# Performance work log

Hardware: AMD Instinct MI355X
Metric: run time of the kernel (lower is better)

## Reference

```python
import jax, jax.numpy as jnp
import numpy as np

B, T, F, H = 1024, 512, 32, 64
EPS = 1e-3  # keras BatchNormalization default epsilon


def lstm_layer(x, Wx, Uh, b):
    """Keras LSTM with activation=relu, recurrent_activation=sigmoid.
    x: [B,T,Fin]; Wx: [Fin,4H]; Uh: [H,4H]; b: [4H]. Gate order i,f,c,o."""
    xz = jnp.einsum('btf,fg->btg', x, Wx) + b  # precompute input projection
    h0 = jnp.zeros((x.shape[0], Uh.shape[0]), x.dtype)

    def step(carry, xz_t):
        h, c = carry
        z = xz_t + h @ Uh
        i, f, g, o = jnp.split(z, 4, axis=-1)
        i = jax.nn.sigmoid(i)
        f = jax.nn.sigmoid(f)
        o = jax.nn.sigmoid(o)
        c = f * c + i * jax.nn.relu(g)
        h = o * jax.nn.relu(c)
        return (h, c), h

    _, hs = jax.lax.scan(step, (h0, h0), jnp.swapaxes(xz, 0, 1))  # [T,B,H]
    return jnp.swapaxes(hs, 0, 1)  # [B,T,H]


def batchnorm(x, gamma, beta, mean, var):
    # inference-mode BN over last axis (keras default axis=-1, training=False)
    return (x - mean) * (gamma * jax.lax.rsqrt(var + EPS)) + beta


def attention(x, W, ht):
    # score = (X @ W) @ h_t -> [B,T]; softmax over time; c_t = X^T @ alpha
    score = jnp.einsum('btd,de,e->bt', x, W, ht[:, 0])
    alpha = jax.nn.softmax(score, axis=1)
    return jnp.einsum('btd,bt->bd', x, alpha)  # [B,H]


def setup_inputs() -> dict:
    key = jax.random.key(0)
    ks = jax.random.split(key, 32)
    d = {'x': jax.random.normal(ks[0], (B, T, F), jnp.float32)}
    fins = [F, H, H]
    for l in range(3):
        fin = fins[l]
        i = l + 1
        d[f'w{i}'] = jax.random.normal(ks[1 + 9 * l], (fin, 4 * H), jnp.float32) * (1.0 / np.sqrt(fin))
        d[f'u{i}'] = jax.random.normal(ks[2 + 9 * l], (H, 4 * H), jnp.float32) * (1.0 / np.sqrt(H))
        d[f'bi{i}'] = jnp.zeros((4 * H,), jnp.float32)
        d[f'gamma{i}'] = jnp.ones((H,), jnp.float32)
        d[f'beta{i}'] = jnp.zeros((H,), jnp.float32)
        d[f'mean{i}'] = jax.random.normal(ks[3 + 9 * l], (H,), jnp.float32) * 0.1
        d[f'var{i}'] = jnp.ones((H,), jnp.float32) + jax.random.uniform(ks[4 + 9 * l], (H,), jnp.float32) * 0.1
        d[f'attw{i}'] = jax.random.truncated_normal(ks[5 + 9 * l], -2, 2, (H, H), jnp.float32) * 0.5
        d[f'attv{i}'] = jax.random.truncated_normal(ks[6 + 9 * l], -2, 2, (H, 1), jnp.float32) * 0.5
    d['dw'] = jax.random.normal(ks[30], (3 * H, 1), jnp.float32) * (1.0 / np.sqrt(3 * H))
    d['db'] = jnp.zeros((1,), jnp.float32)
    return d


def reference(x, w1, u1, bi1, gamma1, beta1, mean1, var1, attw1, attv1,
              w2, u2, bi2, gamma2, beta2, mean2, var2, attw2, attv2,
              w3, u3, bi3, gamma3, beta3, mean3, var3, attw3, attv3,
              dw, db):
    h = lstm_layer(x, w1, u1, bi1)
    h = batchnorm(h, gamma1, beta1, mean1, var1)
    a1 = attention(h, attw1, attv1)
    h = lstm_layer(h, w2, u2, bi2)
    h = batchnorm(h, gamma2, beta2, mean2, var2)
    a2 = attention(h, attw2, attv2)
    h = lstm_layer(h, w3, u3, bi3)
    h = batchnorm(h, gamma3, beta3, mean3, var3)
    a3 = attention(h, attw3, attv3)
    feat = jnp.concatenate([a1, a2, a3], axis=1)  # [B, 3H]
    return feat @ dw + db  # [B, 1]
```

## Files before the change

### kernel.cpp

```cpp
#include <hip/hip_runtime.h>
#include <math.h>

#define BB 1024
#define TT 512
#define FF 32
#define HH 64
#define GG 256
#define TC 64
#define NCHUNK (TT/TC)
#define MB 16
#define NBLK (BB/MB)
#define HPAD 68
#define EPSBN 1e-3f

typedef __attribute__((ext_vector_type(8))) short bf16x8;
typedef __attribute__((ext_vector_type(4))) float f32x4;
typedef __attribute__((ext_vector_type(4))) int   i32x4;

__global__ void fold1_kernel(const float* __restrict__ gamma, const float* __restrict__ beta,
                             const float* __restrict__ mean, const float* __restrict__ var,
                             const float* __restrict__ attw, const float* __restrict__ attv,
                             float* __restrict__ s_out, float* __restrict__ ab_out,
                             float* __restrict__ wv_out) {
    int d = threadIdx.x;
    float s = gamma[d] * rsqrtf(var[d] + EPSBN);
    float ab = beta[d] - mean[d] * s;
    float wvr = 0.f;
    for (int e = 0; e < HH; ++e) wvr += attw[d * HH + e] * attv[e];
    s_out[d] = s;
    ab_out[d] = ab;
    wv_out[d] = s * wvr;
}

__global__ void fold2_kernel(const float* __restrict__ W, const float* __restrict__ b,
                             const float* __restrict__ s_prev, const float* __restrict__ ab_prev,
                             float* __restrict__ Wp, float* __restrict__ bp) {
    int g = threadIdx.x;
    float bacc = b[g];
    for (int d = 0; d < HH; ++d) {
        float w = W[d * GG + g];
        bacc += ab_prev[d] * w;
        Wp[d * GG + g] = s_prev[d] * w;
    }
    bp[g] = bacc;
}

__global__ void init_kernel(float* st_h, float* st_c, float* st_acc, float* st_m, float* st_d) {
    int i = blockIdx.x * blockDim.x + threadIdx.x;
    int n = 3 * BB * HH;
    if (i < n) { st_h[i] = 0.f; st_c[i] = 0.f; st_acc[i] = 0.f; }
    if (i < 3 * BB) { st_m[i] = -3.0e38f; st_d[i] = 0.f; }
}

__device__ __forceinline__ f32x4 ld4(const float* p) { return *reinterpret_cast<const f32x4*>(p); }
__device__ __forceinline__ void st4(float* p, f32x4 v) { *reinterpret_cast<f32x4*>(p) = v; }
__device__ __forceinline__ int cvtpk(float a, float b) {
    int r; asm("v_cvt_pk_bf16_f32 %0, %1, %2" : "=v"(r) : "v"(a), "v"(b)); return r;
}
__device__ __forceinline__ void mkfrag(f32x4 A, f32x4 B, bf16x8& hi, bf16x8& lo) {
    i32x4 H, L;
    H[0] = cvtpk(A[0], A[1]); H[1] = cvtpk(A[2], A[3]);
    H[2] = cvtpk(B[0], B[1]); H[3] = cvtpk(B[2], B[3]);
    L[0] = cvtpk(A[0] - __int_as_float(H[0] << 16), A[1] - __int_as_float(H[0] & 0xffff0000));
    L[1] = cvtpk(A[2] - __int_as_float(H[1] << 16), A[3] - __int_as_float(H[1] & 0xffff0000));
    L[2] = cvtpk(B[0] - __int_as_float(H[2] << 16), B[1] - __int_as_float(H[2] & 0xffff0000));
    L[3] = cvtpk(B[2] - __int_as_float(H[3] << 16), B[3] - __int_as_float(H[3] & 0xffff0000));
    hi = __builtin_bit_cast(bf16x8, H); lo = __builtin_bit_cast(bf16x8, L);
}
__device__ __forceinline__ float sigm(float x) { return __fdividef(1.f, 1.f + __expf(-x)); }
#define MFMA(a, b, c) c = __builtin_amdgcn_mfma_f32_16x16x32_bf16(a, b, c, 0, 0, 0)

struct RecFArgs {
    const float* xin[3]; long sB[3]; long sT[3]; int K[3];
    const float* W[3]; const float* U[3]; const float* bias[3];
    float* Hout[3];
    float* st_h[3]; float* st_c[3]; float* st_acc[3];
    float* st_m[3]; float* st_d[3];
    const float* wv[3]; const float* abv[3]; const float* sbn[3];
    float* a_out[3];
    int last[3]; int first[3];
};

template<int KT>
__device__ __forceinline__ void rec_body(const RecFArgs& A, const int seg, const int b0,
                                         float (*hl)[MB][HPAD]) {
    const int tid = threadIdx.x;
    const int w = tid >> 6;
    const int l = tid & 63;
    const int r = l & 15;
    const int q = l >> 4;
    const int cw = w << 4;

    bf16x8 UHf[4][2], ULf[4][2], WHf[4][KT], WLf[4][KT];
    {
        const float* Up = A.U[seg];
#pragma unroll
        for (int g = 0; g < 4; ++g)
#pragma unroll
            for (int kk = 0; kk < 2; ++kk) {
                const float* p = Up + (size_t)(32 * kk + 8 * q) * GG + 64 * g + cw + r;
                f32x4 a, b;
                a[0] = p[0];      a[1] = p[GG];     a[2] = p[2 * GG]; a[3] = p[3 * GG];
                b[0] = p[4 * GG]; b[1] = p[5 * GG]; b[2] = p[6 * GG]; b[3] = p[7 * GG];
                mkfrag(a, b, UHf[g][kk], ULf[g][kk]);
            }
        const float* Wp = A.W[seg];
#pragma unroll
        for (int g = 0; g < 4; ++g)
#pragma unroll
            for (int kk = 0; kk < KT; ++kk) {
                const float* p = Wp + (size_t)(32 * kk + 8 * q) * GG + 64 * g + cw + r;
                f32x4 a, b;
                a[0] = p[0];      a[1] = p[GG];     a[2] = p[2 * GG]; a[3] = p[3 * GG];
                b[0] = p[4 * GG]; b[1] = p[5 * GG]; b[2] = p[6 * GG]; b[3] = p[7 * GG];
                mkfrag(a, b, WHf[g][kk], WLf[g][kk]);
            }
    }
    f32x4 bias4[4];
#pragma unroll
    for (int g = 0; g < 4; ++g) bias4[g] = ld4(A.bias[seg] + 64 * g + cw + 4 * q);

    f32x4 wva = ld4(A.wv[seg] + 8 * q);
    f32x4 wvb = ld4(A.wv[seg] + 8 * q + 4);
    f32x4 wvc = ld4(A.wv[seg] + 32 + 8 * q);
    f32x4 wvd = ld4(A.wv[seg] + 32 + 8 * q + 4);

    const int grow = b0 + r;
    f32x4 c4   = ld4(A.st_c[seg]   + (size_t)grow * HH + cw + 4 * q);
    f32x4 h4   = ld4(A.st_h[seg]   + (size_t)grow * HH + cw + 4 * q);
    f32x4 acc4 = ld4(A.st_acc[seg] + (size_t)grow * HH + cw + 4 * q);
    float m_b = A.st_m[seg][grow];
    float d_b = A.st_d[seg][grow];

    st4(&hl[0][r][cw + 4 * q], h4);

    const float* xbase = A.xin[seg] + (size_t)grow * A.sB[seg];
    const long sT = A.sT[seg];

    f32x4 XA[2 * KT], XB[2 * KT];
    auto xload = [&](f32x4 (&X)[2 * KT], int t) {
        const float* xp = xbase + (size_t)t * sT + 8 * q;
        X[0] = ld4(xp); X[1] = ld4(xp + 4);
        if constexpr (KT == 2) { X[2] = ld4(xp + 32); X[3] = ld4(xp + 32 + 4); }
    };
    xload(XA, 0);
    xload(XB, 1);

    f32x4 Ca[4], Cb[4];
    auto seedC = [&](f32x4 (&C)[4], f32x4 (&X)[2 * KT]) {
        bf16x8 xh0, xl0, xh1, xl1;
        mkfrag(X[0], X[1], xh0, xl0);
        if constexpr (KT == 2) mkfrag(X[2], X[3], xh1, xl1);
#pragma unroll
        for (int g = 0; g < 4; ++g) {
            C[g] = bias4[g];
            MFMA(WHf[g][0], xh0, C[g]);
            MFMA(WHf[g][0], xl0, C[g]);
            MFMA(WLf[g][0], xh0, C[g]);
            if constexpr (KT == 2) {
                MFMA(WHf[g][1], xh1, C[g]);
                MFMA(WHf[g][1], xl1, C[g]);
                MFMA(WLf[g][1], xh1, C[g]);
            }
        }
    };

    auto attup = [&](int pr) {
        f32x4 f0 = ld4(&hl[pr][r][8 * q]);
        f32x4 f1 = ld4(&hl[pr][r][8 * q + 4]);
        f32x4 f2 = ld4(&hl[pr][r][32 + 8 * q]);
        f32x4 f3 = ld4(&hl[pr][r][32 + 8 * q + 4]);
        float sc = 0.f;
#pragma unroll
        for (int i = 0; i < 4; ++i) {
            sc = fmaf(f0[i], wva[i], sc);
            sc = fmaf(f1[i], wvb[i], sc);
            sc = fmaf(f2[i], wvc[i], sc);
            sc = fmaf(f3[i], wvd[i], sc);
        }
        sc += __shfl_xor(sc, 16);
        sc += __shfl_xor(sc, 32);
        float mn = fmaxf(m_b, sc);
        float corr = __expf(m_b - mn);
        float p = __expf(sc - mn);
        d_b = d_b * corr + p;
        acc4 = acc4 * corr + p * h4;
        m_b = mn;
    };

    float* Hob = A.Hout[seg];
    auto step = [&](int t, f32x4 (&C)[4], int pr, bool do_att) {
        if (Hob && w == 3 && t > 0) {
            const int sr = l >> 2, scol = (l & 3) << 4;
            f32x4 v0 = ld4(&hl[pr][sr][scol]);
            f32x4 v1 = ld4(&hl[pr][sr][scol + 4]);
            f32x4 v2 = ld4(&hl[pr][sr][scol + 8]);
            f32x4 v3 = ld4(&hl[pr][sr][scol + 12]);
            float* op = Hob + (size_t)(b0 + sr) * (TC * HH) + (size_t)(t - 1) * HH + scol;
            st4(op, v0); st4(op + 4, v1); st4(op + 8, v2); st4(op + 12, v3);
        }
        if (do_att) attup(pr);
        f32x4 f0 = ld4(&hl[pr][r][8 * q]);
        f32x4 f1 = ld4(&hl[pr][r][8 * q + 4]);
        f32x4 f2 = ld4(&hl[pr][r][32 + 8 * q]);
        f32x4 f3 = ld4(&hl[pr][r][32 + 8 * q + 4]);
        bf16x8 bh0, bl0, bh1, bl1;
        mkfrag(f0, f1, bh0, bl0);
        mkfrag(f2, f3, bh1, bl1);
#pragma unroll
        for (int g = 0; g < 4; ++g) {
            MFMA(UHf[g][0], bh0, C[g]);
            MFMA(UHf[g][0], bl0, C[g]);
            MFMA(ULf[g][0], bh0, C[g]);
            MFMA(UHf[g][1], bh1, C[g]);
            MFMA(UHf[g][1], bl1, C[g]);
            MFMA(ULf[g][1], bh1, C[g]);
        }
#pragma unroll
        for (int i = 0; i < 4; ++i) {
            float zi = sigm(C[0][i]);
            float zf = sigm(C[1][i]);
            float zg = fmaxf(C[2][i], 0.f);
            float zo = sigm(C[3][i]);
            c4[i] = fmaf(zf, c4[i], zi * zg);
            h4[i] = zo * fmaxf(c4[i], 0.f);
        }
        st4(&hl[pr ^ 1][r][cw + 4 * q], h4);
    };

    const bool first = (A.first[seg] != 0);
    seedC(Ca, XA);
    __syncthreads();

#pragma unroll 1
    for (int it = 0; it < TC / 2; ++it) {
        const int t0 = 2 * it, t1 = 2 * it + 1;
        step(t0, Ca, 0, !(first && t0 == 0));
        xload(XA, (t0 + 2 < TC) ? t0 + 2 : TC - 1);
        seedC(Cb, XB);
        __syncthreads();
        step(t1, Cb, 1, true);
        xload(XB, (t1 + 2 < TC) ? t1 + 2 : TC - 1);
        seedC(Ca, XA);
        __syncthreads();
    }

    if (Hob && w == 3) {
        const int sr = l >> 2, scol = (l & 3) << 4;
        f32x4 v0 = ld4(&hl[0][sr][scol]);
        f32x4 v1 = ld4(&hl[0][sr][scol + 4]);
        f32x4 v2 = ld4(&hl[0][sr][scol + 8]);
        f32x4 v3 = ld4(&hl[0][sr][scol + 12]);
        float* op = Hob + (size_t)(b0 + sr) * (TC * HH) + (size_t)(TC - 1) * HH + scol;
        st4(op, v0); st4(op + 4, v1); st4(op + 8, v2); st4(op + 12, v3);
    }
    if (A.last[seg]) {
        attup(0);
        f32x4 sb = ld4(A.sbn[seg] + cw + 4 * q);
        f32x4 ab = ld4(A.abv[seg] + cw + 4 * q);
        f32x4 res;
#pragma unroll
        for (int i = 0; i < 4; ++i)
            res[i] = sb[i] * __fdividef(acc4[i], d_b) + ab[i];
        st4(A.a_out[seg] + (size_t)grow * HH + cw + 4 * q, res);
    }
    st4(A.st_c[seg]   + (size_t)grow * HH + cw + 4 * q, c4);
    st4(A.st_h[seg]   + (size_t)grow * HH + cw + 4 * q, h4);
    st4(A.st_acc[seg] + (size_t)grow * HH + cw + 4 * q, acc4);
    if (w == 0 && q == 0) { A.st_m[seg][grow] = m_b; A.st_d[seg][grow] = d_b; }
}

__global__ __launch_bounds__(256, 1) void rec_mfma(RecFArgs A) {
    __shared__ float hl[2][MB][HPAD];
    const int seg = blockIdx.x >> 6;
    const int b0 = (blockIdx.x & (NBLK - 1)) << 4;
    if (A.K[seg] == 32) rec_body<1>(A, seg, b0, hl);
    else                rec_body<2>(A, seg, b0, hl);
}

__global__ void final_kernel(const float* __restrict__ a, const float* __restrict__ dw,
                             const float* __restrict__ db, float* __restrict__ out) {
    int b = blockIdx.x * blockDim.x + threadIdx.x;
    if (b >= BB) return;
    float acc = db[0];
    for (int l = 0; l < 3; ++l)
        for (int j = 0; j < HH; ++j)
            acc += a[(l * BB + b) * HH + j] * dw[l * HH + j];
    out[b] = acc;
}

extern "C" void kernel_launch(void* const* d_in, const int* in_sizes, int n_in,
                              void* d_out, int out_size, void* d_ws, size_t ws_size,
                              hipStream_t stream) {
    (void)in_sizes; (void)n_in; (void)out_size; (void)ws_size;
    const float* x = (const float*)d_in[0];
    const float* w[3]    = {(const float*)d_in[1],  (const float*)d_in[10], (const float*)d_in[19]};
    const float* uu[3]   = {(const float*)d_in[2],  (const float*)d_in[11], (const float*)d_in[20]};
    const float* bi[3]   = {(const float*)d_in[3],  (const float*)d_in[12], (const float*)d_in[21]};
    const float* gam[3]  = {(const float*)d_in[4],  (const float*)d_in[13], (const float*)d_in[22]};
    const float* bet[3]  = {(const float*)d_in[5],  (const float*)d_in[14], (const float*)d_in[23]};
    const float* mea[3]  = {(const float*)d_in[6],  (const float*)d_in[15], (const float*)d_in[24]};
    const float* var[3]  = {(const float*)d_in[7],  (const float*)d_in[16], (const float*)d_in[25]};
    const float* atw[3]  = {(const float*)d_in[8],  (const float*)d_in[17], (const float*)d_in[26]};
    const float* atv[3]  = {(const float*)d_in[9],  (const float*)d_in[18], (const float*)d_in[27]};
    const float* dw = (const float*)d_in[28];
    const float* db = (const float*)d_in[29];

    float* ws = (float*)d_ws;
    size_t off = 0;
    float* Hb[2][2];
    for (int l = 0; l < 2; ++l)
        for (int p = 0; p < 2; ++p) { Hb[l][p] = ws + off; off += (size_t)BB * TC * HH; }
    float* st_h  = ws + off; off += 3 * BB * HH;
    float* st_c  = ws + off; off += 3 * BB * HH;
    float* st_ac = ws + off; off += 3 * BB * HH;
    float* st_m  = ws + off; off += 3 * BB;
    float* st_d  = ws + off; off += 3 * BB;
    float* s_ws  = ws + off; off += 3 * HH;
    float* ab_ws = ws + off; off += 3 * HH;
    float* wv_ws = ws + off; off += 3 * HH;
    float* W2p   = ws + off; off += HH * GG;
    float* W3p   = ws + off; off += HH * GG;
    float* b2p   = ws + off; off += GG;
    float* b3p   = ws + off; off += GG;
    float* a_ws  = ws + off; off += 3 * BB * HH;

    for (int l = 0; l < 3; ++l)
        fold1_kernel<<<1, 64, 0, stream>>>(gam[l], bet[l], mea[l], var[l], atw[l], atv[l],
                                           s_ws + l * HH, ab_ws + l * HH, wv_ws + l * HH);
    fold2_kernel<<<1, 256, 0, stream>>>(w[1], bi[1], s_ws + 0 * HH, ab_ws + 0 * HH, W2p, b2p);
    fold2_kernel<<<1, 256, 0, stream>>>(w[2], bi[2], s_ws + 1 * HH, ab_ws + 1 * HH, W3p, b3p);
    init_kernel<<<(3 * BB * HH + 255) / 256, 256, 0, stream>>>(st_h, st_c, st_ac, st_m, st_d);

    const float* Wl[3] = {w[0], W2p, W3p};
    const float* bl[3] = {bi[0], b2p, b3p};

    for (int s = 0; s <= NCHUNK - 1 + 2; ++s) {
        RecFArgs ra;
        int nseg = 0;
        for (int l = 0; l < 3; ++l) {
            int cpos = s - l;
            if (cpos < 0 || cpos >= NCHUNK) continue;
            if (l == 0) {
                ra.xin[nseg] = x + (size_t)cpos * TC * FF;
                ra.sB[nseg] = (long)TT * FF;
                ra.sT[nseg] = FF;
                ra.K[nseg] = 32;
            } else {
                ra.xin[nseg] = Hb[l - 1][(s & 1) ^ 1];
                ra.sB[nseg] = (long)TC * HH;
                ra.sT[nseg] = HH;
                ra.K[nseg] = 64;
            }
            ra.W[nseg] = Wl[l]; ra.U[nseg] = uu[l]; ra.bias[nseg] = bl[l];
            ra.Hout[nseg] = (l < 2) ? Hb[l][s & 1] : (float*)0;
            ra.st_h[nseg] = st_h + l * BB * HH;
            ra.st_c[nseg] = st_c + l * BB * HH;
            ra.st_acc[nseg] = st_ac + l * BB * HH;
            ra.st_m[nseg] = st_m + l * BB;
            ra.st_d[nseg] = st_d + l * BB;
            ra.wv[nseg]  = wv_ws + l * HH;
            ra.abv[nseg] = ab_ws + l * HH;
            ra.sbn[nseg] = s_ws + l * HH;
            ra.a_out[nseg] = a_ws + l * BB * HH;
            ra.last[nseg]  = (cpos == NCHUNK - 1) ? 1 : 0;
            ra.first[nseg] = (cpos == 0) ? 1 : 0;
            ++nseg;
        }
        if (!nseg) continue;
        rec_mfma<<<nseg * NBLK, 256, 0, stream>>>(ra);
    }
    final_kernel<<<(BB + 255) / 256, 256, 0, stream>>>(a_ws, dw, db, (float*)d_out);
}
```

Before: 846.7 us.

## Split recurrence into producer/consumer warps with LDS-staged input projection

The block grows from 256 to 512 threads with warp specialisation. Four consumer warps run only the recurrent h@U MFMAs and the gate nonlinearities. Four producer warps compute the input projection x@W+bias one step ahead into a double-buffered shared-memory array, and they also handle the attention online-softmax update and the write-back of h to global memory. The aim is to take the input projection, attention and store work off the serial recurrence critical path. In exchange it adds shared-memory traffic, an extra LDS read of the gate pre-activations on every step, and heavier per-block resources (launch_bounds 512,2).

```diff
diff --git a/kernel.cpp b/kernel.cpp
--- a/kernel.cpp
+++ b/kernel.cpp
@@ -11,6 +11,7 @@
 #define MB 16
 #define NBLK (BB/MB)
 #define HPAD 68
+#define ZSTRIDE 20
 #define EPSBN 1e-3f
 
 typedef __attribute__((ext_vector_type(8))) short bf16x8;
@@ -83,16 +84,23 @@
 
 template<int KT>
 __device__ __forceinline__ void rec_body(const RecFArgs& A, const int seg, const int b0,
-                                         float (*hl)[MB][HPAD]) {
+                                         float* zx, float (*hl)[MB][HPAD]) {
     const int tid = threadIdx.x;
-    const int w = tid >> 6;
+    const int wall = tid >> 6;
+    const int w = wall & 3;
+    const bool isP = wall >= 4;
     const int l = tid & 63;
     const int r = l & 15;
     const int q = l >> 4;
     const int cw = w << 4;
-
-    bf16x8 UHf[4][2], ULf[4][2], WHf[4][KT], WLf[4][KT];
-    {
+    const int grow = b0 + r;
+
+    auto zxo = [&](int slot, int g) {
+        return (((slot * 4 + w) * 4 + g) * 16 + r) * ZSTRIDE + 4 * q;
+    };
+
+    if (!isP) {
+        bf16x8 UHf[4][2], ULf[4][2];
         const float* Up = A.U[seg];
 #pragma unroll
         for (int g = 0; g < 4; ++g)
@@ -104,6 +112,49 @@
                 b[0] = p[4 * GG]; b[1] = p[5 * GG]; b[2] = p[6 * GG]; b[3] = p[7 * GG];
                 mkfrag(a, b, UHf[g][kk], ULf[g][kk]);
             }
+        f32x4 c4 = ld4(A.st_c[seg] + (size_t)grow * HH + cw + 4 * q);
+        f32x4 h4 = ld4(A.st_h[seg] + (size_t)grow * HH + cw + 4 * q);
+        st4(&hl[0][r][cw + 4 * q], h4);
+        __syncthreads();
+
+#pragma unroll 1
+        for (int t = 0; t < TC; ++t) {
+            const int pr = t & 1;
+            f32x4 C[4];
+#pragma unroll
+            for (int g = 0; g < 4; ++g) C[g] = ld4(zx + zxo(pr, g));
+            f32x4 f0 = ld4(&hl[pr][r][8 * q]);
+            f32x4 f1 = ld4(&hl[pr][r][8 * q + 4]);
+            f32x4 f2 = ld4(&hl[pr][r][32 + 8 * q]);
+            f32x4 f3 = ld4(&hl[pr][r][32 + 8 * q + 4]);
+            bf16x8 bh0, bl0, bh1, bl1;
+            mkfrag(f0, f1, bh0, bl0);
+            mkfrag(f2, f3, bh1, bl1);
+#pragma unroll
+            for (int g = 0; g < 4; ++g) {
+                MFMA(UHf[g][0], bh0, C[g]);
+                MFMA(UHf[g][0], bl0, C[g]);
+                MFMA(ULf[g][0], bh0, C[g]);
+                MFMA(UHf[g][1], bh1, C[g]);
+                MFMA(UHf[g][1], bl1, C[g]);
+                MFMA(ULf[g][1], bh1, C[g]);
+            }
+#pragma unroll
+            for (int i = 0; i < 4; ++i) {
+                float zi = sigm(C[0][i]);
+                float zf = sigm(C[1][i]);
+                float zg = fmaxf(C[2][i], 0.f);
+                float zo = sigm(C[3][i]);
+                c4[i] = fmaf(zf, c4[i], zi * zg);
+                h4[i] = zo * fmaxf(c4[i], 0.f);
+            }
+            st4(&hl[pr ^ 1][r][cw + 4 * q], h4);
+            __syncthreads();
+        }
+        st4(A.st_c[seg] + (size_t)grow * HH + cw + 4 * q, c4);
+        st4(A.st_h[seg] + (size_t)grow * HH + cw + 4 * q, h4);
+    } else {
+        bf16x8 WHf[4][KT], WLf[4][KT];
         const float* Wp = A.W[seg];
 #pragma unroll
         for (int g = 0; g < 4; ++g)
@@ -115,167 +166,117 @@
                 b[0] = p[4 * GG]; b[1] = p[5 * GG]; b[2] = p[6 * GG]; b[3] = p[7 * GG];
                 mkfrag(a, b, WHf[g][kk], WLf[g][kk]);
             }
+        f32x4 bias4[4];
+#pragma unroll
+        for (int g = 0; g < 4; ++g) bias4[g] = ld4(A.bias[seg] + 64 * g + cw + 4 * q);
+        f32x4 wva = ld4(A.wv[seg] + 8 * q);
+        f32x4 wvb = ld4(A.wv[seg] + 8 * q + 4);
+        f32x4 wvc = ld4(A.wv[seg] + 32 + 8 * q);
+        f32x4 wvd = ld4(A.wv[seg] + 32 + 8 * q + 4);
+        f32x4 acc4 = ld4(A.st_acc[seg] + (size_t)grow * HH + cw + 4 * q);
+        float m_b = A.st_m[seg][grow];
+        float d_b = A.st_d[seg][grow];
+
+        const float* xbase = A.xin[seg] + (size_t)grow * A.sB[seg];
+        const long sT = A.sT[seg];
+        auto xload = [&](f32x4 (&X)[2 * KT], int t) {
+            const float* xp = xbase + (size_t)t * sT + 8 * q;
+            X[0] = ld4(xp); X[1] = ld4(xp + 4);
+            if constexpr (KT == 2) { X[2] = ld4(xp + 32); X[3] = ld4(xp + 32 + 4); }
+        };
+        auto produce = [&](int slot, f32x4 (&X)[2 * KT]) {
+            bf16x8 xh0, xl0, xh1, xl1;
+            mkfrag(X[0], X[1], xh0, xl0);
+            if constexpr (KT == 2) mkfrag(X[2], X[3], xh1, xl1);
+#pragma unroll
+            for (int g = 0; g < 4; ++g) {
+                f32x4 Cx = bias4[g];
+                MFMA(WHf[g][0], xh0, Cx);
+                MFMA(WHf[g][0], xl0, Cx);
+                MFMA(WLf[g][0], xh0, Cx);
+                if constexpr (KT == 2) {
+                    MFMA(WHf[g][1], xh1, Cx);
+                    MFMA(WHf[g][1], xl1, Cx);
+                    MFMA(WLf[g][1], xh1, Cx);
+                }
+                st4(zx + zxo(slot, g), Cx);
+            }
+        };
+        auto attup = [&](int pr) {
+            f32x4 f0 = ld4(&hl[pr][r][8 * q]);
+            f32x4 f1 = ld4(&hl[pr][r][8 * q + 4]);
+            f32x4 f2 = ld4(&hl[pr][r][32 + 8 * q]);
+            f32x4 f3 = ld4(&hl[pr][r][32 + 8 * q + 4]);
+            float sc = 0.f;
+#pragma unroll
+            for (int i = 0; i < 4; ++i) {
+                sc = fmaf(f0[i], wva[i], sc);
+                sc = fmaf(f1[i], wvb[i], sc);
+                sc = fmaf(f2[i], wvc[i], sc);
+                sc = fmaf(f3[i], wvd[i], sc);
+            }
+            sc += __shfl_xor(sc, 16);
+            sc += __shfl_xor(sc, 32);
+            f32x4 hp4 = ld4(&hl[pr][r][cw + 4 * q]);
+            float mn = fmaxf(m_b, sc);
+            float corr = __expf(m_b - mn);
+            float p = __expf(sc - mn);
+            d_b = d_b * corr + p;
+            acc4 = acc4 * corr + p * hp4;
+            m_b = mn;
+        };
+        float* Hob = A.Hout[seg];
+        auto stage = [&](int pr, int tt) {
+            const int sr = (w << 2) + q;
+            f32x4 v = ld4(&hl[pr][sr][4 * r]);
+            st4(Hob + (size_t)(b0 + sr) * (TC * HH) + (size_t)tt * HH + 4 * r, v);
+        };
+
+        f32x4 X0[2 * KT], XA[2 * KT], XB[2 * KT];
+        xload(X0, 0);
+        produce(0, X0);
+        xload(XA, 1);
+        xload(XB, 2 < TC ? 2 : TC - 1);
+        __syncthreads();
+
+        const bool first = A.first[seg] != 0;
+#pragma unroll 1
+        for (int t = 0; t < TC; ++t) {
+            const int pr = t & 1;
+            if (t + 1 < TC) {
+                if (pr == 0) produce(1, XA); else produce(0, XB);
+            }
+            {
+                int tn = t + 3 < TC ? t + 3 : TC - 1;
+                if (pr == 0) xload(XA, tn); else xload(XB, tn);
+            }
+            if (!(first && t == 0)) attup(pr);
+            if (Hob && t > 0) stage(pr, t - 1);
+            __syncthreads();
+        }
+        if (Hob) stage(0, TC - 1);
+        if (A.last[seg]) attup(0);
+        st4(A.st_acc[seg] + (size_t)grow * HH + cw + 4 * q, acc4);
+        if (w == 0 && q == 0) { A.st_m[seg][grow] = m_b; A.st_d[seg][grow] = d_b; }
+        if (A.last[seg]) {
+            f32x4 sb = ld4(A.sbn[seg] + cw + 4 * q);
+            f32x4 ab = ld4(A.abv[seg] + cw + 4 * q);
+            f32x4 res;
+#pragma unroll
+            for (int i = 0; i < 4; ++i)
+                res[i] = sb[i] * __fdividef(acc4[i], d_b) + ab[i];
+            st4(A.a_out[seg] + (size_t)grow * HH + cw + 4 * q, res);
+        }
     }
-    f32x4 bias4[4];
-#pragma unroll
-    for (int g = 0; g < 4; ++g) bias4[g] = ld4(A.bias[seg] + 64 * g + cw + 4 * q);
-
-    f32x4 wva = ld4(A.wv[seg] + 8 * q);
-    f32x4 wvb = ld4(A.wv[seg] + 8 * q + 4);
-    f32x4 wvc = ld4(A.wv[seg] + 32 + 8 * q);
-    f32x4 wvd = ld4(A.wv[seg] + 32 + 8 * q + 4);
-
-    const int grow = b0 + r;
-    f32x4 c4   = ld4(A.st_c[seg]   + (size_t)grow * HH + cw + 4 * q);
-    f32x4 h4   = ld4(A.st_h[seg]   + (size_t)grow * HH + cw + 4 * q);
-    f32x4 acc4 = ld4(A.st_acc[seg] + (size_t)grow * HH + cw + 4 * q);
-    float m_b = A.st_m[seg][grow];
-    float d_b = A.st_d[seg][grow];
-
-    st4(&hl[0][r][cw + 4 * q], h4);
-
-    const float* xbase = A.xin[seg] + (size_t)grow * A.sB[seg];
-    const long sT = A.sT[seg];
-
-    f32x4 XA[2 * KT], XB[2 * KT];
-    auto xload = [&](f32x4 (&X)[2 * KT], int t) {
-        const float* xp = xbase + (size_t)t * sT + 8 * q;
-        X[0] = ld4(xp); X[1] = ld4(xp + 4);
-        if constexpr (KT == 2) { X[2] = ld4(xp + 32); X[3] = ld4(xp + 32 + 4); }
-    };
-    xload(XA, 0);
-    xload(XB, 1);
-
-    f32x4 Ca[4], Cb[4];
-    auto seedC = [&](f32x4 (&C)[4], f32x4 (&X)[2 * KT]) {
-        bf16x8 xh0, xl0, xh1, xl1;
-        mkfrag(X[0], X[1], xh0, xl0);
-        if constexpr (KT == 2) mkfrag(X[2], X[3], xh1, xl1);
-#pragma unroll
-        for (int g = 0; g < 4; ++g) {
-            C[g] = bias4[g];
-            MFMA(WHf[g][0], xh0, C[g]);
-            MFMA(WHf[g][0], xl0, C[g]);
-            MFMA(WLf[g][0], xh0, C[g]);
-            if constexpr (KT == 2) {
-                MFMA(WHf[g][1], xh1, C[g]);
-                MFMA(WHf[g][1], xl1, C[g]);
-                MFMA(WLf[g][1], xh1, C[g]);
-            }
-        }
-    };
-
-    auto attup = [&](int pr) {
-        f32x4 f0 = ld4(&hl[pr][r][8 * q]);
-        f32x4 f1 = ld4(&hl[pr][r][8 * q + 4]);
-        f32x4 f2 = ld4(&hl[pr][r][32 + 8 * q]);
-        f32x4 f3 = ld4(&hl[pr][r][32 + 8 * q + 4]);
-        float sc = 0.f;
-#pragma unroll
-        for (int i = 0; i < 4; ++i) {
-            sc = fmaf(f0[i], wva[i], sc);
-            sc = fmaf(f1[i], wvb[i], sc);
-            sc = fmaf(f2[i], wvc[i], sc);
-            sc = fmaf(f3[i], wvd[i], sc);
-        }
-        sc += __shfl_xor(sc, 16);
-        sc += __shfl_xor(sc, 32);
-        float mn = fmaxf(m_b, sc);
-        float corr = __expf(m_b - mn);
-        float p = __expf(sc - mn);
-        d_b = d_b * corr + p;
-        acc4 = acc4 * corr + p * h4;
-        m_b = mn;
-    };
-
-    float* Hob = A.Hout[seg];
-    auto step = [&](int t, f32x4 (&C)[4], int pr, bool do_att) {
-        if (Hob && w == 3 && t > 0) {
-            const int sr = l >> 2, scol = (l & 3) << 4;
-            f32x4 v0 = ld4(&hl[pr][sr][scol]);
-            f32x4 v1 = ld4(&hl[pr][sr][scol + 4]);
-            f32x4 v2 = ld4(&hl[pr][sr][scol + 8]);
-            f32x4 v3 = ld4(&hl[pr][sr][scol + 12]);
-            float* op = Hob + (size_t)(b0 + sr) * (TC * HH) + (size_t)(t - 1) * HH + scol;
-            st4(op, v0); st4(op + 4, v1); st4(op + 8, v2); st4(op + 12, v3);
-        }
-        if (do_att) attup(pr);
-        f32x4 f0 = ld4(&hl[pr][r][8 * q]);
-        f32x4 f1 = ld4(&hl[pr][r][8 * q + 4]);
-        f32x4 f2 = ld4(&hl[pr][r][32 + 8 * q]);
-        f32x4 f3 = ld4(&hl[pr][r][32 + 8 * q + 4]);
-        bf16x8 bh0, bl0, bh1, bl1;
-        mkfrag(f0, f1, bh0, bl0);
-        mkfrag(f2, f3, bh1, bl1);
-#pragma unroll
-        for (int g = 0; g < 4; ++g) {
-            MFMA(UHf[g][0], bh0, C[g]);
-            MFMA(UHf[g][0], bl0, C[g]);
-            MFMA(ULf[g][0], bh0, C[g]);
-            MFMA(UHf[g][1], bh1, C[g]);
-            MFMA(UHf[g][1], bl1, C[g]);
-            MFMA(ULf[g][1], bh1, C[g]);
-        }
-#pragma unroll
-        for (int i = 0; i < 4; ++i) {
-            float zi = sigm(C[0][i]);
-            float zf = sigm(C[1][i]);
-            float zg = fmaxf(C[2][i], 0.f);
-            float zo = sigm(C[3][i]);
-            c4[i] = fmaf(zf, c4[i], zi * zg);
-            h4[i] = zo * fmaxf(c4[i], 0.f);
-        }
-        st4(&hl[pr ^ 1][r][cw + 4 * q], h4);
-    };
-
-    const bool first = (A.first[seg] != 0);
-    seedC(Ca, XA);
-    __syncthreads();
-
-#pragma unroll 1
-    for (int it = 0; it < TC / 2; ++it) {
-        const int t0 = 2 * it, t1 = 2 * it + 1;
-        step(t0, Ca, 0, !(first && t0 == 0));
-        xload(XA, (t0 + 2 < TC) ? t0 + 2 : TC - 1);
-        seedC(Cb, XB);
-        __syncthreads();
-        step(t1, Cb, 1, true);
-        xload(XB, (t1 + 2 < TC) ? t1 + 2 : TC - 1);
-        seedC(Ca, XA);
-        __syncthreads();
-    }
-
-    if (Hob && w == 3) {
-        const int sr = l >> 2, scol = (l & 3) << 4;
-        f32x4 v0 = ld4(&hl[0][sr][scol]);
-        f32x4 v1 = ld4(&hl[0][sr][scol + 4]);
-        f32x4 v2 = ld4(&hl[0][sr][scol + 8]);
-        f32x4 v3 = ld4(&hl[0][sr][scol + 12]);
-        float* op = Hob + (size_t)(b0 + sr) * (TC * HH) + (size_t)(TC - 1) * HH + scol;
-        st4(op, v0); st4(op + 4, v1); st4(op + 8, v2); st4(op + 12, v3);
-    }
-    if (A.last[seg]) {
-        attup(0);
-        f32x4 sb = ld4(A.sbn[seg] + cw + 4 * q);
-        f32x4 ab = ld4(A.abv[seg] + cw + 4 * q);
-        f32x4 res;
-#pragma unroll
-        for (int i = 0; i < 4; ++i)
-            res[i] = sb[i] * __fdividef(acc4[i], d_b) + ab[i];
-        st4(A.a_out[seg] + (size_t)grow * HH + cw + 4 * q, res);
-    }
-    st4(A.st_c[seg]   + (size_t)grow * HH + cw + 4 * q, c4);
-    st4(A.st_h[seg]   + (size_t)grow * HH + cw + 4 * q, h4);
-    st4(A.st_acc[seg] + (size_t)grow * HH + cw + 4 * q, acc4);
-    if (w == 0 && q == 0) { A.st_m[seg][grow] = m_b; A.st_d[seg][grow] = d_b; }
-}
-
-__global__ __launch_bounds__(256, 1) void rec_mfma(RecFArgs A) {
+}
+
+__global__ __launch_bounds__(512, 2) void rec_pc(RecFArgs A) {
+    __shared__ float zx[2 * 4 * 4 * 16 * ZSTRIDE];
     __shared__ float hl[2][MB][HPAD];
     const int seg = blockIdx.x >> 6;
     const int b0 = (blockIdx.x & (NBLK - 1)) << 4;
-    if (A.K[seg] == 32) rec_body<1>(A, seg, b0, hl);
-    else                rec_body<2>(A, seg, b0, hl);
+    if (A.K[seg] == 32) rec_body<1>(A, seg, b0, zx, hl);
+    else                rec_body<2>(A, seg, b0, zx, hl);
 }
 
 __global__ void final_kernel(const float* __restrict__ a, const float* __restrict__ dw,
@@ -368,7 +369,7 @@
             ++nseg;
         }
         if (!nseg) continue;
-        rec_mfma<<<nseg * NBLK, 256, 0, stream>>>(ra);
+        rec_pc<<<nseg * NBLK, 512, 0, stream>>>(ra);
     }
     final_kernel<<<(BB + 255) / 256, 256, 0, stream>>>(a_ws, dw, db, (float*)d_out);
 }
```

Measured after the change: 1.075 ms. 1.27x slower.

## Precompute bf16 weight fragments and restructure recurrent step pipeline with direct H stores

Applied to the files above, without the earlier changes.

Adds a prep kernel that converts U and W into hi/lo bf16 MFMA fragments once, so each recurrent block loads prepacked fragments instead of strided fp32 loads plus conversion on every launch. The step loop is rewritten into a single STEP lambda: it seeds the next step's input projection and prefetches x three steps ahead, and it reuses the loaded h fragments for the attention update. Each thread now writes its h directly to global memory instead of wave 3 copying the previous step's h from LDS. This aims to cut per-launch setup cost and shorten the serial critical path, but it adds extra launches, more workspace, and more register pressure from holding an extra x buffer.

```diff
diff --git a/kernel.cpp b/kernel.cpp
--- a/kernel.cpp
+++ b/kernel.cpp
@@ -16,6 +16,7 @@
 typedef __attribute__((ext_vector_type(8))) short bf16x8;
 typedef __attribute__((ext_vector_type(4))) float f32x4;
 typedef __attribute__((ext_vector_type(4))) int   i32x4;
+typedef unsigned short ushort_t;
 
 __global__ void fold1_kernel(const float* __restrict__ gamma, const float* __restrict__ beta,
                              const float* __restrict__ mean, const float* __restrict__ var,
@@ -70,9 +71,28 @@
 __device__ __forceinline__ float sigm(float x) { return __fdividef(1.f, 1.f + __expf(-x)); }
 #define MFMA(a, b, c) c = __builtin_amdgcn_mfma_f32_16x16x32_bf16(a, b, c, 0, 0, 0)
 
+__global__ void prep_frags(const float* __restrict__ M, int KT, ushort_t* __restrict__ outF) {
+    int idx = blockIdx.x * 256 + threadIdx.x;
+    int tot = 16 * KT * 512;
+    if (idx >= tot) return;
+    int e = idx & 7, l = (idx >> 3) & 63, f = idx >> 9;
+    int kt = f % KT, gw = f / KT;
+    int g = gw & 3, w = gw >> 2;
+    int r = l & 15, q = l >> 4;
+    int k = 32 * kt + 8 * q + e;
+    int col = 64 * g + 16 * w + r;
+    float v = M[(size_t)k * GG + col];
+    int hb = cvtpk(v, v) & 0xffff;
+    float hf = __int_as_float(hb << 16);
+    float lo = v - hf;
+    int lb = cvtpk(lo, lo) & 0xffff;
+    outF[(size_t)(f * 2 + 0) * 512 + l * 8 + e] = (ushort_t)hb;
+    outF[(size_t)(f * 2 + 1) * 512 + l * 8 + e] = (ushort_t)lb;
+}
+
 struct RecFArgs {
     const float* xin[3]; long sB[3]; long sT[3]; int K[3];
-    const float* W[3]; const float* U[3]; const float* bias[3];
+    const ushort_t* UF[3]; const ushort_t* WF[3]; const float* bias[3];
     float* Hout[3];
     float* st_h[3]; float* st_c[3]; float* st_acc[3];
     float* st_m[3]; float* st_d[3];
@@ -90,42 +110,34 @@
     const int r = l & 15;
     const int q = l >> 4;
     const int cw = w << 4;
-
+    const int grow = b0 + r;
+
+    const bf16x8* UF = reinterpret_cast<const bf16x8*>(A.UF[seg]);
+    const bf16x8* WF = reinterpret_cast<const bf16x8*>(A.WF[seg]);
     bf16x8 UHf[4][2], ULf[4][2], WHf[4][KT], WLf[4][KT];
-    {
-        const float* Up = A.U[seg];
-#pragma unroll
-        for (int g = 0; g < 4; ++g)
-#pragma unroll
-            for (int kk = 0; kk < 2; ++kk) {
-                const float* p = Up + (size_t)(32 * kk + 8 * q) * GG + 64 * g + cw + r;
-                f32x4 a, b;
-                a[0] = p[0];      a[1] = p[GG];     a[2] = p[2 * GG]; a[3] = p[3 * GG];
-                b[0] = p[4 * GG]; b[1] = p[5 * GG]; b[2] = p[6 * GG]; b[3] = p[7 * GG];
-                mkfrag(a, b, UHf[g][kk], ULf[g][kk]);
-            }
-        const float* Wp = A.W[seg];
-#pragma unroll
-        for (int g = 0; g < 4; ++g)
-#pragma unroll
-            for (int kk = 0; kk < KT; ++kk) {
-                const float* p = Wp + (size_t)(32 * kk + 8 * q) * GG + 64 * g + cw + r;
-                f32x4 a, b;
-                a[0] = p[0];      a[1] = p[GG];     a[2] = p[2 * GG]; a[3] = p[3 * GG];
-                b[0] = p[4 * GG]; b[1] = p[5 * GG]; b[2] = p[6 * GG]; b[3] = p[7 * GG];
-                mkfrag(a, b, WHf[g][kk], WLf[g][kk]);
-            }
+#pragma unroll
+    for (int g = 0; g < 4; ++g) {
+#pragma unroll
+        for (int kt = 0; kt < 2; ++kt) {
+            const int fU = (w * 4 + g) * 2 + kt;
+            UHf[g][kt] = UF[(fU * 2 + 0) * 64 + l];
+            ULf[g][kt] = UF[(fU * 2 + 1) * 64 + l];
+        }
+#pragma unroll
+        for (int kt = 0; kt < KT; ++kt) {
+            const int fW = (w * 4 + g) * KT + kt;
+            WHf[g][kt] = WF[(fW * 2 + 0) * 64 + l];
+            WLf[g][kt] = WF[(fW * 2 + 1) * 64 + l];
+        }
     }
     f32x4 bias4[4];
 #pragma unroll
     for (int g = 0; g < 4; ++g) bias4[g] = ld4(A.bias[seg] + 64 * g + cw + 4 * q);
-
     f32x4 wva = ld4(A.wv[seg] + 8 * q);
     f32x4 wvb = ld4(A.wv[seg] + 8 * q + 4);
     f32x4 wvc = ld4(A.wv[seg] + 32 + 8 * q);
     f32x4 wvd = ld4(A.wv[seg] + 32 + 8 * q + 4);
 
-    const int grow = b0 + r;
     f32x4 c4   = ld4(A.st_c[seg]   + (size_t)grow * HH + cw + 4 * q);
     f32x4 h4   = ld4(A.st_h[seg]   + (size_t)grow * HH + cw + 4 * q);
     f32x4 acc4 = ld4(A.st_acc[seg] + (size_t)grow * HH + cw + 4 * q);
@@ -137,17 +149,12 @@
     const float* xbase = A.xin[seg] + (size_t)grow * A.sB[seg];
     const long sT = A.sT[seg];
 
-    f32x4 XA[2 * KT], XB[2 * KT];
     auto xload = [&](f32x4 (&X)[2 * KT], int t) {
         const float* xp = xbase + (size_t)t * sT + 8 * q;
         X[0] = ld4(xp); X[1] = ld4(xp + 4);
         if constexpr (KT == 2) { X[2] = ld4(xp + 32); X[3] = ld4(xp + 32 + 4); }
     };
-    xload(XA, 0);
-    xload(XB, 1);
-
-    f32x4 Ca[4], Cb[4];
-    auto seedC = [&](f32x4 (&C)[4], f32x4 (&X)[2 * KT]) {
+    auto seed = [&](f32x4 (&C)[4], f32x4 (&X)[2 * KT]) {
         bf16x8 xh0, xl0, xh1, xl1;
         mkfrag(X[0], X[1], xh0, xl0);
         if constexpr (KT == 2) mkfrag(X[2], X[3], xh1, xl1);
@@ -164,12 +171,7 @@
             }
         }
     };
-
-    auto attup = [&](int pr) {
-        f32x4 f0 = ld4(&hl[pr][r][8 * q]);
-        f32x4 f1 = ld4(&hl[pr][r][8 * q + 4]);
-        f32x4 f2 = ld4(&hl[pr][r][32 + 8 * q]);
-        f32x4 f3 = ld4(&hl[pr][r][32 + 8 * q + 4]);
+    auto attup = [&](f32x4 f0, f32x4 f1, f32x4 f2, f32x4 f3, f32x4 hp4) {
         float sc = 0.f;
 #pragma unroll
         for (int i = 0; i < 4; ++i) {
@@ -184,78 +186,69 @@
         float corr = __expf(m_b - mn);
         float p = __expf(sc - mn);
         d_b = d_b * corr + p;
-        acc4 = acc4 * corr + p * h4;
+        acc4 = acc4 * corr + p * hp4;
         m_b = mn;
     };
 
+    f32x4 XA[2 * KT], XB[2 * KT];
+    f32x4 Ca[4], Cb[4];
+    xload(XA, 0);
+    seed(Ca, XA);
+    xload(XA, 1);
+    xload(XB, 2);
+    __syncthreads();
+
+    const bool first = A.first[seg] != 0;
     float* Hob = A.Hout[seg];
-    auto step = [&](int t, f32x4 (&C)[4], int pr, bool do_att) {
-        if (Hob && w == 3 && t > 0) {
-            const int sr = l >> 2, scol = (l & 3) << 4;
-            f32x4 v0 = ld4(&hl[pr][sr][scol]);
-            f32x4 v1 = ld4(&hl[pr][sr][scol + 4]);
-            f32x4 v2 = ld4(&hl[pr][sr][scol + 8]);
-            f32x4 v3 = ld4(&hl[pr][sr][scol + 12]);
-            float* op = Hob + (size_t)(b0 + sr) * (TC * HH) + (size_t)(t - 1) * HH + scol;
-            st4(op, v0); st4(op + 4, v1); st4(op + 8, v2); st4(op + 12, v3);
-        }
-        if (do_att) attup(pr);
+
+    auto STEP = [&](int t, f32x4 (&Cc)[4], f32x4 (&Cn)[4], f32x4 (&X)[2 * KT]) {
+        const int pr = t & 1;
         f32x4 f0 = ld4(&hl[pr][r][8 * q]);
         f32x4 f1 = ld4(&hl[pr][r][8 * q + 4]);
         f32x4 f2 = ld4(&hl[pr][r][32 + 8 * q]);
         f32x4 f3 = ld4(&hl[pr][r][32 + 8 * q + 4]);
+        f32x4 hp4 = ld4(&hl[pr][r][cw + 4 * q]);
         bf16x8 bh0, bl0, bh1, bl1;
         mkfrag(f0, f1, bh0, bl0);
         mkfrag(f2, f3, bh1, bl1);
 #pragma unroll
         for (int g = 0; g < 4; ++g) {
-            MFMA(UHf[g][0], bh0, C[g]);
-            MFMA(UHf[g][0], bl0, C[g]);
-            MFMA(ULf[g][0], bh0, C[g]);
-            MFMA(UHf[g][1], bh1, C[g]);
-            MFMA(UHf[g][1], bl1, C[g]);
-            MFMA(ULf[g][1], bh1, C[g]);
-        }
+            MFMA(UHf[g][0], bh0, Cc[g]);
+            MFMA(UHf[g][0], bl0, Cc[g]);
+            MFMA(ULf[g][0], bh0, Cc[g]);
+            MFMA(UHf[g][1], bh1, Cc[g]);
+            MFMA(UHf[g][1], bl1, Cc[g]);
+            MFMA(ULf[g][1], bh1, Cc[g]);
+        }
+        seed(Cn, X);
+        if (!(first && t == 0)) attup(f0, f1, f2, f3, hp4);
+        { int tn = t + 3 < TC ? t + 3 : TC - 1; xload(X, tn); }
 #pragma unroll
         for (int i = 0; i < 4; ++i) {
-            float zi = sigm(C[0][i]);
-            float zf = sigm(C[1][i]);
-            float zg = fmaxf(C[2][i], 0.f);
-            float zo = sigm(C[3][i]);
+            float zi = sigm(Cc[0][i]);
+            float zf = sigm(Cc[1][i]);
+            float zg = fmaxf(Cc[2][i], 0.f);
+            float zo = sigm(Cc[3][i]);
             c4[i] = fmaf(zf, c4[i], zi * zg);
             h4[i] = zo * fmaxf(c4[i], 0.f);
         }
         st4(&hl[pr ^ 1][r][cw + 4 * q], h4);
+        if (Hob) st4(Hob + (size_t)grow * (TC * HH) + (size_t)t * HH + cw + 4 * q, h4);
+        __syncthreads();
     };
-
-    const bool first = (A.first[seg] != 0);
-    seedC(Ca, XA);
-    __syncthreads();
 
 #pragma unroll 1
     for (int it = 0; it < TC / 2; ++it) {
-        const int t0 = 2 * it, t1 = 2 * it + 1;
-        step(t0, Ca, 0, !(first && t0 == 0));
-        xload(XA, (t0 + 2 < TC) ? t0 + 2 : TC - 1);
-        seedC(Cb, XB);
-        __syncthreads();
-        step(t1, Cb, 1, true);
-        xload(XB, (t1 + 2 < TC) ? t1 + 2 : TC - 1);
-        seedC(Ca, XA);
-        __syncthreads();
-    }
-
-    if (Hob && w == 3) {
-        const int sr = l >> 2, scol = (l & 3) << 4;
-        f32x4 v0 = ld4(&hl[0][sr][scol]);
-        f32x4 v1 = ld4(&hl[0][sr][scol + 4]);
-        f32x4 v2 = ld4(&hl[0][sr][scol + 8]);
-        f32x4 v3 = ld4(&hl[0][sr][scol + 12]);
-        float* op = Hob + (size_t)(b0 + sr) * (TC * HH) + (size_t)(TC - 1) * HH + scol;
-        st4(op, v0); st4(op + 4, v1); st4(op + 8, v2); st4(op + 12, v3);
-    }
+        STEP(2 * it,     Ca, Cb, XA);
+        STEP(2 * it + 1, Cb, Ca, XB);
+    }
+
     if (A.last[seg]) {
-        attup(0);
+        f32x4 f0 = ld4(&hl[0][r][8 * q]);
+        f32x4 f1 = ld4(&hl[0][r][8 * q + 4]);
+        f32x4 f2 = ld4(&hl[0][r][32 + 8 * q]);
+        f32x4 f3 = ld4(&hl[0][r][32 + 8 * q + 4]);
+        attup(f0, f1, f2, f3, h4);
         f32x4 sb = ld4(A.sbn[seg] + cw + 4 * q);
         f32x4 ab = ld4(A.abv[seg] + cw + 4 * q);
         f32x4 res;
@@ -324,6 +317,9 @@
     float* b2p   = ws + off; off += GG;
     float* b3p   = ws + off; off += GG;
     float* a_ws  = ws + off; off += 3 * BB * HH;
+    ushort_t* UFb[3]; ushort_t* WFb[3];
+    for (int l = 0; l < 3; ++l) { UFb[l] = (ushort_t*)(ws + off); off += 16384; }
+    for (int l = 0; l < 3; ++l) { WFb[l] = (ushort_t*)(ws + off); off += 16384; }
 
     for (int l = 0; l < 3; ++l)
         fold1_kernel<<<1, 64, 0, stream>>>(gam[l], bet[l], mea[l], var[l], atw[l], atv[l],
@@ -332,7 +328,12 @@
     fold2_kernel<<<1, 256, 0, stream>>>(w[2], bi[2], s_ws + 1 * HH, ab_ws + 1 * HH, W3p, b3p);
     init_kernel<<<(3 * BB * HH + 255) / 256, 256, 0, stream>>>(st_h, st_c, st_ac, st_m, st_d);
 
-    const float* Wl[3] = {w[0], W2p, W3p};
+    for (int l = 0; l < 3; ++l)
+        prep_frags<<<64, 256, 0, stream>>>(uu[l], 2, UFb[l]);
+    prep_frags<<<32, 256, 0, stream>>>(w[0], 1, WFb[0]);
+    prep_frags<<<64, 256, 0, stream>>>(W2p, 2, WFb[1]);
+    prep_frags<<<64, 256, 0, stream>>>(W3p, 2, WFb[2]);
+
     const float* bl[3] = {bi[0], b2p, b3p};
 
     for (int s = 0; s <= NCHUNK - 1 + 2; ++s) {
@@ -352,7 +353,7 @@
                 ra.sT[nseg] = HH;
                 ra.K[nseg] = 64;
             }
-            ra.W[nseg] = Wl[l]; ra.U[nseg] = uu[l]; ra.bias[nseg] = bl[l];
+            ra.UF[nseg] = UFb[l]; ra.WF[nseg] = WFb[l]; ra.bias[nseg] = bl[l];
             ra.Hout[nseg] = (l < 2) ? Hb[l][s & 1] : (float*)0;
             ra.st_h[nseg] = st_h + l * BB * HH;
             ra.st_c[nseg] = st_c + l * BB * HH;
```

Measured after the change: 800.2 us. -5.5%, faster.
